# Optimization experiments

Measured on AMD Instinct MI355X. Metric: run time of the kernel, lower is better.

The kernel has to match this reference:

```python
import jax, jax.numpy as jnp
import numpy as np

I, T, Q, K, E, H = 16, 64, 196, 32, 512, 8
D = E // H


def setup_inputs() -> dict:
    key = jax.random.key(0)
    ks = jax.random.split(key, 8)
    image = jax.random.normal(ks[0], (I, Q, E), dtype=jnp.float32)
    text = jax.random.normal(ks[1], (T, K, E), dtype=jnp.float32)
    text_mask = jax.random.randint(ks[2], (T, K), 0, 2).astype(bool)
    text_mask = text_mask.at[:, 0].set(True)  # avoid fully-masked rows
    s = 1.0 / np.sqrt(D)
    Wq = jax.random.normal(ks[3], (D, D), dtype=jnp.float32) * s
    Wk = jax.random.normal(ks[4], (D, D), dtype=jnp.float32) * s
    Wv = jax.random.normal(ks[5], (D, D), dtype=jnp.float32) * s
    Wo = jax.random.normal(ks[6], (E, E), dtype=jnp.float32) * (1.0 / np.sqrt(E))
    bo = jnp.zeros((E,), dtype=jnp.float32)
    return {"image": image, "text": text, "text_mask": text_mask,
            "Wq": Wq, "Wk": Wk, "Wv": Wv, "Wo": Wo, "bo": bo}


def reference(image, text, text_mask, Wq, Wk, Wv, Wo, bo):
    i, q_len, e = image.shape
    t, k_len, _ = text.shape
    img = image.reshape(i, q_len, H, D)   # i q h d
    txt = text.reshape(t, k_len, H, D)    # t k h d
    # torch Linear: x @ W.T (bias=False for q/k/v)
    query = jnp.einsum('iqhd,ed->iqhe', img, Wq)
    key_p = jnp.einsum('tkhd,ed->tkhe', txt, Wk)
    value = jnp.einsum('tkhd,ed->tkhe', txt, Wv)
    energy = jnp.einsum('tkhd,iqhd->ithqk', key_p, query)
    neg = jnp.finfo(jnp.float32).min
    energy = jnp.where(text_mask[None, :, None, None, :], energy, neg)
    scaled = energy / (e ** 0.5)
    attention = jax.nn.softmax(scaled, axis=-1)        # over k
    text_attention = jax.nn.softmax(scaled, axis=-2)   # over q
    out = jnp.einsum('ithqk,tkhd->itqhd', attention, value)
    out = out.reshape(i, t, q_len, e)                  # i t q (h d)
    out = jnp.einsum('itqe,fe->itqf', out, Wo) + bo    # fc_out
    out = out.mean(axis=2)                             # pooling_type='mean'
    return out, attention, text_attention
```

## Files before the change

kernel.cpp:

```cpp
#include <hip/hip_runtime.h>
#include <math.h>

#define I_N 16
#define T_N 64
#define Q_N 196
#define K_N 32
#define E_N 512
#define H_N 8
#define D_N 64

#define INV_SQRT_E (0.044194173824159216f)

typedef __attribute__((ext_vector_type(8))) short bf16x8;
typedef __attribute__((ext_vector_type(4))) float f32x4;

__device__ __forceinline__ short f2bf(float x) {
    unsigned u = __builtin_bit_cast(unsigned, x);
    unsigned r = (u + 0x7fffu + ((u >> 16) & 1u)) >> 16;
    return (short)r;
}
__device__ __forceinline__ float bf2f(short s) {
    unsigned u = ((unsigned)(unsigned short)s) << 16;
    return __builtin_bit_cast(float, u);
}

__global__ __launch_bounds__(512) void detect_mask_kernel(const unsigned int* __restrict__ mask,
                                                          int* __restrict__ flag) {
    __shared__ int notSimple, sawFloat;
    int tid = threadIdx.x;
    if (tid == 0) { notSimple = 0; sawFloat = 0; }
    __syncthreads();
    unsigned int v = mask[tid];
    if (v != 0u && v != 1u && v != 0x3f800000u) atomicOr(&notSimple, 1);
    if (v == 0x3f800000u) atomicOr(&sawFloat, 1);
    __syncthreads();
    if (tid == 0) flag[0] = notSimple ? 2 : (sawFloat ? 1 : 0);
}

__global__ __launch_bounds__(256) void proj_q_kernel(const float* __restrict__ x,
                                                     const float* __restrict__ W,
                                                     unsigned short* __restrict__ qh,
                                                     unsigned short* __restrict__ ql) {
    __shared__ float sWt[64 * 65];
    __shared__ float sX[16 * 64];
    int tid = threadIdx.x;
    for (int j = tid; j < 4096; j += 256) {
        int n = j >> 6, d = j & 63;
        sWt[d * 65 + n] = W[j];
    }
    int rowBase = blockIdx.x * 16;
    for (int j = tid; j < 1024; j += 256) sX[j] = x[rowBase * 64 + j];
    __syncthreads();
    int wave = tid >> 6, lane = tid & 63;
    float acc[4] = {0.f, 0.f, 0.f, 0.f};
    for (int d = 0; d < 64; ++d) {
        float w = sWt[d * 65 + lane];
#pragma unroll
        for (int j = 0; j < 4; ++j) acc[j] += sX[(wave * 4 + j) * 64 + d] * w;
    }
#pragma unroll
    for (int j = 0; j < 4; ++j) {
        int r = rowBase + wave * 4 + j;
        int i = r / (Q_N * H_N);
        int rem = r - i * (Q_N * H_N);
        int q = rem >> 3, h = rem & 7;
        size_t dst = (((size_t)i * H_N + h) * Q_N + q) * 64 + lane;
        float a = acc[j] * INV_SQRT_E;
        short hi = f2bf(a);
        qh[dst] = (unsigned short)hi;
        ql[dst] = (unsigned short)f2bf(a - bf2f(hi));
    }
}

__global__ __launch_bounds__(256) void proj_kv_kernel(const float* __restrict__ x,
                                                      const float* __restrict__ Wk,
                                                      const float* __restrict__ Wv,
                                                      unsigned short* __restrict__ kh,
                                                      unsigned short* __restrict__ kl,
                                                      float* __restrict__ vout) {
    __shared__ float sWkT[64 * 65];
    __shared__ float sWvT[64 * 65];
    __shared__ float sX[16 * 64];
    int tid = threadIdx.x;
    for (int j = tid; j < 4096; j += 256) {
        int n = j >> 6, d = j & 63;
        sWkT[d * 65 + n] = Wk[j];
        sWvT[d * 65 + n] = Wv[j];
    }
    int rowBase = blockIdx.x * 16;
    for (int j = tid; j < 1024; j += 256) sX[j] = x[rowBase * 64 + j];
    __syncthreads();
    int wave = tid >> 6, lane = tid & 63;
    float ak[4] = {0.f, 0.f, 0.f, 0.f};
    float av[4] = {0.f, 0.f, 0.f, 0.f};
    for (int d = 0; d < 64; ++d) {
        float wk = sWkT[d * 65 + lane];
        float wv = sWvT[d * 65 + lane];
#pragma unroll
        for (int j = 0; j < 4; ++j) {
            float xv = sX[(wave * 4 + j) * 64 + d];
            ak[j] += xv * wk;
            av[j] += xv * wv;
        }
    }
#pragma unroll
    for (int j = 0; j < 4; ++j) {
        int r = rowBase + wave * 4 + j;
        int t = r >> 8;
        int rem = r & 255;
        int k = rem >> 3, h = rem & 7;
        size_t dst = (((size_t)t * H_N + h) * K_N + k) * 64 + lane;
        short hi = f2bf(ak[j]);
        kh[dst] = (unsigned short)hi;
        kl[dst] = (unsigned short)f2bf(ak[j] - bf2f(hi));
        vout[dst] = av[j];
    }
}

__global__ __launch_bounds__(256) void transpose_wo_kernel(const float* __restrict__ Wo,
                                                           float* __restrict__ WoT) {
    __shared__ float tile[32][33];
    int tx = threadIdx.x & 31, ty = threadIdx.x >> 5;
    int e0 = blockIdx.x * 32, f0 = blockIdx.y * 32;
#pragma unroll
    for (int k = 0; k < 4; ++k) {
        int fy = ty + k * 8;
        tile[fy][tx] = Wo[(size_t)(f0 + fy) * E_N + e0 + tx];
    }
    __syncthreads();
#pragma unroll
    for (int k = 0; k < 4; ++k) {
        int ey = ty + k * 8;
        WoT[(size_t)(e0 + ey) * E_N + f0 + tx] = tile[tx][ey];
    }
}

__global__ __launch_bounds__(256) void attn_kernel(const unsigned short* __restrict__ qhi,
                                                   const unsigned short* __restrict__ qlo,
                                                   const unsigned short* __restrict__ khi,
                                                   const unsigned short* __restrict__ klo,
                                                   const float* __restrict__ vproj,
                                                   const int* __restrict__ mask,
                                                   const int* __restrict__ modeFlag,
                                                   float* __restrict__ attn_out,
                                                   float* __restrict__ tattn_out,
                                                   float* __restrict__ pooled) {
    __shared__ float sS[Q_N * 33];
    __shared__ float sRrow[Q_N];
    __shared__ float sColS[4 * 32];
    __shared__ float sCaW[4 * 32];
    __shared__ float sColR[32];
    __shared__ float sCa[32];
    __shared__ float sMask[K_N];

    int tid = threadIdx.x;
    int bid = blockIdx.x;
    int h = bid & 7;
    int t = (bid >> 3) & 63;
    int i = bid >> 9;
    int lane = tid & 63, wave = tid >> 6;
    int quad = lane >> 4, lid = lane & 15;

    int mode = modeFlag[0];
    if (tid < K_N) {
        int idx = t * K_N + tid;
        bool keep;
        if (mode == 2)      keep = ((const unsigned char*)mask)[idx] != 0;
        else if (mode == 1) keep = ((const float*)mask)[idx] != 0.0f;
        else                keep = mask[idx] != 0;
        sMask[tid] = keep ? 1.0f : 0.0f;
    }
    __syncthreads();

    size_t kbase = ((size_t)t * H_N + h) * (K_N * 64);
    bf16x8 Bh[2][2], Bl[2][2];
#pragma unroll
    for (int nt = 0; nt < 2; ++nt)
#pragma unroll
        for (int ks = 0; ks < 2; ++ks) {
            size_t off = kbase + (size_t)(nt * 16 + lid) * 64 + ks * 32 + quad * 8;
            Bh[nt][ks] = *(const bf16x8*)(khi + off);
            Bl[nt][ks] = *(const bf16x8*)(klo + off);
        }

    float keep0 = sMask[lid], keep1 = sMask[16 + lid];
    size_t qoff = ((size_t)i * H_N + h) * (Q_N * 64);

    float cs0 = 0.f, cs1 = 0.f;

    for (int mt = wave; mt < 13; mt += 4) {
        int qb = mt * 16;
        int qr = qb + lid; if (qr > Q_N - 1) qr = Q_N - 1;
        const unsigned short* ph = qhi + qoff + (size_t)qr * 64 + quad * 8;
        const unsigned short* pl = qlo + qoff + (size_t)qr * 64 + quad * 8;
        bf16x8 Ah0 = *(const bf16x8*)ph;
        bf16x8 Ah1 = *(const bf16x8*)(ph + 32);
        bf16x8 Al0 = *(const bf16x8*)pl;
        bf16x8 Al1 = *(const bf16x8*)(pl + 32);

        f32x4 acc0 = {0.f, 0.f, 0.f, 0.f}, acc1 = {0.f, 0.f, 0.f, 0.f};
        acc0 = __builtin_amdgcn_mfma_f32_16x16x32_bf16(Al0, Bh[0][0], acc0, 0, 0, 0);
        acc0 = __builtin_amdgcn_mfma_f32_16x16x32_bf16(Ah0, Bl[0][0], acc0, 0, 0, 0);
        acc0 = __builtin_amdgcn_mfma_f32_16x16x32_bf16(Ah0, Bh[0][0], acc0, 0, 0, 0);
        acc0 = __builtin_amdgcn_mfma_f32_16x16x32_bf16(Al1, Bh[0][1], acc0, 0, 0, 0);
        acc0 = __builtin_amdgcn_mfma_f32_16x16x32_bf16(Ah1, Bl[0][1], acc0, 0, 0, 0);
        acc0 = __builtin_amdgcn_mfma_f32_16x16x32_bf16(Ah1, Bh[0][1], acc0, 0, 0, 0);
        acc1 = __builtin_amdgcn_mfma_f32_16x16x32_bf16(Al0, Bh[1][0], acc1, 0, 0, 0);
        acc1 = __builtin_amdgcn_mfma_f32_16x16x32_bf16(Ah0, Bl[1][0], acc1, 0, 0, 0);
        acc1 = __builtin_amdgcn_mfma_f32_16x16x32_bf16(Ah0, Bh[1][0], acc1, 0, 0, 0);
        acc1 = __builtin_amdgcn_mfma_f32_16x16x32_bf16(Al1, Bh[1][1], acc1, 0, 0, 0);
        acc1 = __builtin_amdgcn_mfma_f32_16x16x32_bf16(Ah1, Bl[1][1], acc1, 0, 0, 0);
        acc1 = __builtin_amdgcn_mfma_f32_16x16x32_bf16(Ah1, Bh[1][1], acc1, 0, 0, 0);

#pragma unroll
        for (int reg = 0; reg < 4; ++reg) {
            int q = qb + quad * 4 + reg;
            bool valid = q < Q_N;
            float p0 = keep0 * __expf(acc0[reg]);
            float p1 = keep1 * __expf(acc1[reg]);
            if (valid) {
                sS[q * 33 + lid] = p0;
                sS[q * 33 + 16 + lid] = p1;
                cs0 += p0;
                cs1 += p1;
            }
            float rs = p0 + p1;
            rs += __shfl_xor(rs, 1);
            rs += __shfl_xor(rs, 2);
            rs += __shfl_xor(rs, 4);
            rs += __shfl_xor(rs, 8);
            if (valid && lid == 0) sRrow[q] = 1.0f / rs;
        }
    }
    cs0 += __shfl_xor(cs0, 16);
    cs0 += __shfl_xor(cs0, 32);
    cs1 += __shfl_xor(cs1, 16);
    cs1 += __shfl_xor(cs1, 32);
    if (lane < 16) {
        sColS[wave * 32 + lid] = cs0;
        sColS[wave * 32 + 16 + lid] = cs1;
    }
    __syncthreads();

    if (tid < 32) {
        float s = sColS[tid] + sColS[32 + tid] + sColS[64 + tid] + sColS[96 + tid];
        sColR[tid] = s > 0.f ? 1.0f / s : -1.0f;
    }
    __syncthreads();

    const float invQ = 1.0f / 196.0f;
    int rowt = tid >> 3, kg = tid & 7;
    float cr[4];
#pragma unroll
    for (int c = 0; c < 4; ++c) cr[c] = sColR[kg * 4 + c];
    float ca[4] = {0.f, 0.f, 0.f, 0.f};
    float* ab = attn_out + (size_t)bid * (Q_N * K_N);
    float* tb = tattn_out + (size_t)bid * (Q_N * K_N);
#pragma unroll
    for (int j = 0; j < 7; ++j) {
        int qq = rowt + 32 * j;
        if (qq < Q_N) {
            float rr = sRrow[qq];
            const float* rp = &sS[qq * 33 + kg * 4];
            float p0 = rp[0], p1 = rp[1], p2 = rp[2], p3 = rp[3];
            f32x4 av = {p0 * rr, p1 * rr, p2 * rr, p3 * rr};
            ca[0] += av[0]; ca[1] += av[1]; ca[2] += av[2]; ca[3] += av[3];
            f32x4 tv = {cr[0] < 0.f ? invQ : p0 * cr[0],
                        cr[1] < 0.f ? invQ : p1 * cr[1],
                        cr[2] < 0.f ? invQ : p2 * cr[2],
                        cr[3] < 0.f ? invQ : p3 * cr[3]};
            __builtin_nontemporal_store(av, (f32x4*)(ab + qq * 32 + kg * 4));
            __builtin_nontemporal_store(tv, (f32x4*)(tb + qq * 32 + kg * 4));
        }
    }
#pragma unroll
    for (int c = 0; c < 4; ++c) {
        ca[c] += __shfl_xor(ca[c], 8);
        ca[c] += __shfl_xor(ca[c], 16);
        ca[c] += __shfl_xor(ca[c], 32);
    }
    if (lane < 8) {
#pragma unroll
        for (int c = 0; c < 4; ++c) sCaW[wave * 32 + lane * 4 + c] = ca[c];
    }
    __syncthreads();
    if (tid < 32) sCa[tid] = sCaW[tid] + sCaW[32 + tid] + sCaW[64 + tid] + sCaW[96 + tid];
    __syncthreads();

    if (tid < 64) {
        const float* vb = vproj + kbase + tid;
        float acc = 0.f;
#pragma unroll
        for (int k = 0; k < K_N; ++k) acc += sCa[k] * vb[k * 64];
        pooled[((size_t)(i * T_N + t)) * E_N + h * 64 + tid] = acc;
    }
}

__global__ __launch_bounds__(256) void fc_out_kernel(const float* __restrict__ pooled,
                                                     const float* __restrict__ WoT,
                                                     const float* __restrict__ bo,
                                                     float* __restrict__ out) {
    __shared__ float sPT[E_N * 4];
    int tid = threadIdx.x;
    int p0 = blockIdx.x * 4;
#pragma unroll
    for (int j = 0; j < 4; ++j) {
        sPT[tid * 4 + j] = pooled[(size_t)(p0 + j) * E_N + tid];
        sPT[(256 + tid) * 4 + j] = pooled[(size_t)(p0 + j) * E_N + 256 + tid];
    }
    __syncthreads();
    const float4* sPT4 = (const float4*)sPT;
    int f = blockIdx.y * 256 + tid;
    float4 acc = make_float4(0.f, 0.f, 0.f, 0.f);
    for (int e = 0; e < E_N; e += 2) {
        float w0 = WoT[(size_t)e * E_N + f];
        float w1 = WoT[(size_t)(e + 1) * E_N + f];
        float4 pv0 = sPT4[e];
        float4 pv1 = sPT4[e + 1];
        acc.x += pv0.x * w0 + pv1.x * w1;
        acc.y += pv0.y * w0 + pv1.y * w1;
        acc.z += pv0.z * w0 + pv1.z * w1;
        acc.w += pv0.w * w0 + pv1.w * w1;
    }
    const float invQ = 1.0f / 196.0f;
    float b = bo[f];
    out[(size_t)(p0 + 0) * E_N + f] = b + acc.x * invQ;
    out[(size_t)(p0 + 1) * E_N + f] = b + acc.y * invQ;
    out[(size_t)(p0 + 2) * E_N + f] = b + acc.z * invQ;
    out[(size_t)(p0 + 3) * E_N + f] = b + acc.w * invQ;
}

extern "C" void kernel_launch(void* const* d_in, const int* in_sizes, int n_in,
                              void* d_out, int out_size, void* d_ws, size_t ws_size,
                              hipStream_t stream) {
    const float* image = (const float*)d_in[0];
    const float* text  = (const float*)d_in[1];
    const int*   mask  = (const int*)d_in[2];
    const float* Wq    = (const float*)d_in[3];
    const float* Wk    = (const float*)d_in[4];
    const float* Wv    = (const float*)d_in[5];
    const float* Wo    = (const float*)d_in[6];
    const float* bo    = (const float*)d_in[7];
    float* out = (float*)d_out;

    unsigned short* qhi = (unsigned short*)d_ws;
    unsigned short* qlo = qhi + (size_t)I_N * Q_N * H_N * D_N;
    unsigned short* khi = qlo + (size_t)I_N * Q_N * H_N * D_N;
    unsigned short* klo = khi + (size_t)T_N * K_N * H_N * D_N;
    float* vproj  = (float*)(klo + (size_t)T_N * K_N * H_N * D_N);
    float* pooled = vproj + (size_t)T_N * K_N * H_N * D_N;
    float* WoT    = pooled + (size_t)I_N * T_N * E_N;
    int*   mode   = (int*)(WoT + (size_t)E_N * E_N);

    float* attn  = out + (size_t)I_N * T_N * E_N;
    float* tattn = attn + (size_t)I_N * T_N * H_N * Q_N * K_N;

    detect_mask_kernel<<<1, 512, 0, stream>>>((const unsigned int*)mask, mode);
    proj_q_kernel<<<(I_N * Q_N * H_N) / 16, 256, 0, stream>>>(image, Wq, qhi, qlo);
    proj_kv_kernel<<<(T_N * K_N * H_N) / 16, 256, 0, stream>>>(text, Wk, Wv, khi, klo, vproj);
    transpose_wo_kernel<<<dim3(16, 16), 256, 0, stream>>>(Wo, WoT);
    attn_kernel<<<I_N * T_N * H_N, 256, 0, stream>>>(qhi, qlo, khi, klo, vproj, mask, mode,
                                                     attn, tattn, pooled);
    fc_out_kernel<<<dim3((I_N * T_N) / 4, 2), 256, 0, stream>>>(pooled, WoT, bo, out);
}
```

Before: 508.3 us.

## Merge prep kernels into one launch and write attention inside softmax loop

Folds the mask detection, Q projection, K/V projection and Wo transpose into a single prep kernel that dispatches on block index, so three kernel launches go away. In the attention kernel, the row-softmax normalisation and the attention store now happen directly in the MMA/exp loop, with the column sums of attention accumulated in registers. This drops the per-row reciprocal array in shared memory and one pair of barriers. The trade-off is that attention rows are now written as scalar per-lane stores instead of f32x4 vectors. The merged kernel also reserves the largest shared-memory footprint for every block, which may lower occupancy for the Q-projection blocks.

```diff
diff --git a/kernel.cpp b/kernel.cpp
--- a/kernel.cpp
+++ b/kernel.cpp
@@ -24,114 +24,122 @@
     return __builtin_bit_cast(float, u);
 }
 
-__global__ __launch_bounds__(512) void detect_mask_kernel(const unsigned int* __restrict__ mask,
-                                                          int* __restrict__ flag) {
-    __shared__ int notSimple, sawFloat;
-    int tid = threadIdx.x;
-    if (tid == 0) { notSimple = 0; sawFloat = 0; }
-    __syncthreads();
-    unsigned int v = mask[tid];
-    if (v != 0u && v != 1u && v != 0x3f800000u) atomicOr(&notSimple, 1);
-    if (v == 0x3f800000u) atomicOr(&sawFloat, 1);
-    __syncthreads();
-    if (tid == 0) flag[0] = notSimple ? 2 : (sawFloat ? 1 : 0);
-}
-
-__global__ __launch_bounds__(256) void proj_q_kernel(const float* __restrict__ x,
-                                                     const float* __restrict__ W,
-                                                     unsigned short* __restrict__ qh,
-                                                     unsigned short* __restrict__ ql) {
-    __shared__ float sWt[64 * 65];
-    __shared__ float sX[16 * 64];
-    int tid = threadIdx.x;
-    for (int j = tid; j < 4096; j += 256) {
-        int n = j >> 6, d = j & 63;
-        sWt[d * 65 + n] = W[j];
-    }
-    int rowBase = blockIdx.x * 16;
-    for (int j = tid; j < 1024; j += 256) sX[j] = x[rowBase * 64 + j];
-    __syncthreads();
-    int wave = tid >> 6, lane = tid & 63;
-    float acc[4] = {0.f, 0.f, 0.f, 0.f};
-    for (int d = 0; d < 64; ++d) {
-        float w = sWt[d * 65 + lane];
-#pragma unroll
-        for (int j = 0; j < 4; ++j) acc[j] += sX[(wave * 4 + j) * 64 + d] * w;
-    }
-#pragma unroll
-    for (int j = 0; j < 4; ++j) {
-        int r = rowBase + wave * 4 + j;
-        int i = r / (Q_N * H_N);
-        int rem = r - i * (Q_N * H_N);
-        int q = rem >> 3, h = rem & 7;
-        size_t dst = (((size_t)i * H_N + h) * Q_N + q) * 64 + lane;
-        float a = acc[j] * INV_SQRT_E;
-        short hi = f2bf(a);
-        qh[dst] = (unsigned short)hi;
-        ql[dst] = (unsigned short)f2bf(a - bf2f(hi));
-    }
-}
-
-__global__ __launch_bounds__(256) void proj_kv_kernel(const float* __restrict__ x,
-                                                      const float* __restrict__ Wk,
-                                                      const float* __restrict__ Wv,
-                                                      unsigned short* __restrict__ kh,
-                                                      unsigned short* __restrict__ kl,
-                                                      float* __restrict__ vout) {
-    __shared__ float sWkT[64 * 65];
-    __shared__ float sWvT[64 * 65];
-    __shared__ float sX[16 * 64];
-    int tid = threadIdx.x;
-    for (int j = tid; j < 4096; j += 256) {
-        int n = j >> 6, d = j & 63;
-        sWkT[d * 65 + n] = Wk[j];
-        sWvT[d * 65 + n] = Wv[j];
-    }
-    int rowBase = blockIdx.x * 16;
-    for (int j = tid; j < 1024; j += 256) sX[j] = x[rowBase * 64 + j];
-    __syncthreads();
-    int wave = tid >> 6, lane = tid & 63;
-    float ak[4] = {0.f, 0.f, 0.f, 0.f};
-    float av[4] = {0.f, 0.f, 0.f, 0.f};
-    for (int d = 0; d < 64; ++d) {
-        float wk = sWkT[d * 65 + lane];
-        float wv = sWvT[d * 65 + lane];
+#define PQ_BLOCKS 1568
+#define PKV_BLOCKS 1024
+#define TW_BLOCKS 256
+#define PREP_GRID (PQ_BLOCKS + PKV_BLOCKS + TW_BLOCKS + 1)
+
+__global__ __launch_bounds__(256) void prep_kernel(const float* __restrict__ image,
+                                                   const float* __restrict__ Wq,
+                                                   const float* __restrict__ text,
+                                                   const float* __restrict__ Wk,
+                                                   const float* __restrict__ Wv,
+                                                   const float* __restrict__ Wo,
+                                                   const unsigned int* __restrict__ mask,
+                                                   unsigned short* __restrict__ qh,
+                                                   unsigned short* __restrict__ ql,
+                                                   unsigned short* __restrict__ kh,
+                                                   unsigned short* __restrict__ kl,
+                                                   float* __restrict__ vout,
+                                                   float* __restrict__ WoT,
+                                                   int* __restrict__ flag) {
+    __shared__ float smem[2 * 4160 + 1024];
+    int bid = blockIdx.x, tid = threadIdx.x;
+
+    if (bid < PQ_BLOCKS) {
+        float* sWt = smem;
+        float* sX  = smem + 4160;
+        for (int j = tid; j < 4096; j += 256) {
+            int n = j >> 6, d = j & 63;
+            sWt[d * 65 + n] = Wq[j];
+        }
+        int rowBase = bid * 16;
+        for (int j = tid; j < 1024; j += 256) sX[j] = image[rowBase * 64 + j];
+        __syncthreads();
+        int wave = tid >> 6, lane = tid & 63;
+        float acc[4] = {0.f, 0.f, 0.f, 0.f};
+        for (int d = 0; d < 64; ++d) {
+            float w = sWt[d * 65 + lane];
+#pragma unroll
+            for (int j = 0; j < 4; ++j) acc[j] += sX[(wave * 4 + j) * 64 + d] * w;
+        }
 #pragma unroll
         for (int j = 0; j < 4; ++j) {
-            float xv = sX[(wave * 4 + j) * 64 + d];
-            ak[j] += xv * wk;
-            av[j] += xv * wv;
-        }
-    }
-#pragma unroll
-    for (int j = 0; j < 4; ++j) {
-        int r = rowBase + wave * 4 + j;
-        int t = r >> 8;
-        int rem = r & 255;
-        int k = rem >> 3, h = rem & 7;
-        size_t dst = (((size_t)t * H_N + h) * K_N + k) * 64 + lane;
-        short hi = f2bf(ak[j]);
-        kh[dst] = (unsigned short)hi;
-        kl[dst] = (unsigned short)f2bf(ak[j] - bf2f(hi));
-        vout[dst] = av[j];
-    }
-}
-
-__global__ __launch_bounds__(256) void transpose_wo_kernel(const float* __restrict__ Wo,
-                                                           float* __restrict__ WoT) {
-    __shared__ float tile[32][33];
-    int tx = threadIdx.x & 31, ty = threadIdx.x >> 5;
-    int e0 = blockIdx.x * 32, f0 = blockIdx.y * 32;
-#pragma unroll
-    for (int k = 0; k < 4; ++k) {
-        int fy = ty + k * 8;
-        tile[fy][tx] = Wo[(size_t)(f0 + fy) * E_N + e0 + tx];
-    }
-    __syncthreads();
-#pragma unroll
-    for (int k = 0; k < 4; ++k) {
-        int ey = ty + k * 8;
-        WoT[(size_t)(e0 + ey) * E_N + f0 + tx] = tile[tx][ey];
+            int r = rowBase + wave * 4 + j;
+            int i = r / (Q_N * H_N);
+            int rem = r - i * (Q_N * H_N);
+            int q = rem >> 3, h = rem & 7;
+            size_t dst = (((size_t)i * H_N + h) * Q_N + q) * 64 + lane;
+            float a = acc[j] * INV_SQRT_E;
+            short hi = f2bf(a);
+            qh[dst] = (unsigned short)hi;
+            ql[dst] = (unsigned short)f2bf(a - bf2f(hi));
+        }
+    } else if (bid < PQ_BLOCKS + PKV_BLOCKS) {
+        float* sWkT = smem;
+        float* sWvT = smem + 4160;
+        float* sX   = smem + 8320;
+        for (int j = tid; j < 4096; j += 256) {
+            int n = j >> 6, d = j & 63;
+            sWkT[d * 65 + n] = Wk[j];
+            sWvT[d * 65 + n] = Wv[j];
+        }
+        int rowBase = (bid - PQ_BLOCKS) * 16;
+        for (int j = tid; j < 1024; j += 256) sX[j] = text[rowBase * 64 + j];
+        __syncthreads();
+        int wave = tid >> 6, lane = tid & 63;
+        float ak[4] = {0.f, 0.f, 0.f, 0.f};
+        float av[4] = {0.f, 0.f, 0.f, 0.f};
+        for (int d = 0; d < 64; ++d) {
+            float wk = sWkT[d * 65 + lane];
+            float wv = sWvT[d * 65 + lane];
+#pragma unroll
+            for (int j = 0; j < 4; ++j) {
+                float xv = sX[(wave * 4 + j) * 64 + d];
+                ak[j] += xv * wk;
+                av[j] += xv * wv;
+            }
+        }
+#pragma unroll
+        for (int j = 0; j < 4; ++j) {
+            int r = rowBase + wave * 4 + j;
+            int t = r >> 8;
+            int rem = r & 255;
+            int k = rem >> 3, h = rem & 7;
+            size_t dst = (((size_t)t * H_N + h) * K_N + k) * 64 + lane;
+            short hi = f2bf(ak[j]);
+            kh[dst] = (unsigned short)hi;
+            kl[dst] = (unsigned short)f2bf(ak[j] - bf2f(hi));
+            vout[dst] = av[j];
+        }
+    } else if (bid < PQ_BLOCKS + PKV_BLOCKS + TW_BLOCKS) {
+        float (*tile)[33] = (float (*)[33])smem;
+        int b = bid - (PQ_BLOCKS + PKV_BLOCKS);
+        int tx = tid & 31, ty = tid >> 5;
+        int e0 = (b & 15) * 32, f0 = (b >> 4) * 32;
+#pragma unroll
+        for (int k = 0; k < 4; ++k) {
+            int fy = ty + k * 8;
+            tile[fy][tx] = Wo[(size_t)(f0 + fy) * E_N + e0 + tx];
+        }
+        __syncthreads();
+#pragma unroll
+        for (int k = 0; k < 4; ++k) {
+            int ey = ty + k * 8;
+            WoT[(size_t)(e0 + ey) * E_N + f0 + tx] = tile[tx][ey];
+        }
+    } else {
+        int* fl = (int*)smem;
+        if (tid == 0) { fl[0] = 0; fl[1] = 0; }
+        __syncthreads();
+#pragma unroll
+        for (int j = 0; j < 2; ++j) {
+            unsigned int v = mask[tid + j * 256];
+            if (v != 0u && v != 1u && v != 0x3f800000u) atomicOr(&fl[0], 1);
+            if (v == 0x3f800000u) atomicOr(&fl[1], 1);
+        }
+        __syncthreads();
+        if (tid == 0) flag[0] = fl[0] ? 2 : (fl[1] ? 1 : 0);
     }
 }
 
@@ -146,7 +154,6 @@
                                                    float* __restrict__ tattn_out,
                                                    float* __restrict__ pooled) {
     __shared__ float sS[Q_N * 33];
-    __shared__ float sRrow[Q_N];
     __shared__ float sColS[4 * 32];
     __shared__ float sCaW[4 * 32];
     __shared__ float sColR[32];
@@ -185,8 +192,10 @@
 
     float keep0 = sMask[lid], keep1 = sMask[16 + lid];
     size_t qoff = ((size_t)i * H_N + h) * (Q_N * 64);
+    float* ab = attn_out + (size_t)bid * (Q_N * K_N);
 
     float cs0 = 0.f, cs1 = 0.f;
+    float ca0 = 0.f, ca1 = 0.f;
 
     for (int mt = wave; mt < 13; mt += 4) {
         int qb = mt * 16;
@@ -218,33 +227,41 @@
             bool valid = q < Q_N;
             float p0 = keep0 * __expf(acc0[reg]);
             float p1 = keep1 * __expf(acc1[reg]);
+            float rs = p0 + p1;
+            rs += __shfl_xor(rs, 1);
+            rs += __shfl_xor(rs, 2);
+            rs += __shfl_xor(rs, 4);
+            rs += __shfl_xor(rs, 8);
+            float rr = 1.0f / rs;
             if (valid) {
                 sS[q * 33 + lid] = p0;
                 sS[q * 33 + 16 + lid] = p1;
                 cs0 += p0;
                 cs1 += p1;
+                float a0 = p0 * rr, a1 = p1 * rr;
+                ca0 += a0;
+                ca1 += a1;
+                __builtin_nontemporal_store(a0, ab + q * 32 + lid);
+                __builtin_nontemporal_store(a1, ab + q * 32 + 16 + lid);
             }
-            float rs = p0 + p1;
-            rs += __shfl_xor(rs, 1);
-            rs += __shfl_xor(rs, 2);
-            rs += __shfl_xor(rs, 4);
-            rs += __shfl_xor(rs, 8);
-            if (valid && lid == 0) sRrow[q] = 1.0f / rs;
-        }
-    }
-    cs0 += __shfl_xor(cs0, 16);
-    cs0 += __shfl_xor(cs0, 32);
-    cs1 += __shfl_xor(cs1, 16);
-    cs1 += __shfl_xor(cs1, 32);
+        }
+    }
+    cs0 += __shfl_xor(cs0, 16);  cs0 += __shfl_xor(cs0, 32);
+    cs1 += __shfl_xor(cs1, 16);  cs1 += __shfl_xor(cs1, 32);
+    ca0 += __shfl_xor(ca0, 16);  ca0 += __shfl_xor(ca0, 32);
+    ca1 += __shfl_xor(ca1, 16);  ca1 += __shfl_xor(ca1, 32);
     if (lane < 16) {
         sColS[wave * 32 + lid] = cs0;
         sColS[wave * 32 + 16 + lid] = cs1;
+        sCaW[wave * 32 + lid] = ca0;
+        sCaW[wave * 32 + 16 + lid] = ca1;
     }
     __syncthreads();
 
     if (tid < 32) {
         float s = sColS[tid] + sColS[32 + tid] + sColS[64 + tid] + sColS[96 + tid];
         sColR[tid] = s > 0.f ? 1.0f / s : -1.0f;
+        sCa[tid] = sCaW[tid] + sCaW[32 + tid] + sCaW[64 + tid] + sCaW[96 + tid];
     }
     __syncthreads();
 
@@ -253,39 +270,20 @@
     float cr[4];
 #pragma unroll
     for (int c = 0; c < 4; ++c) cr[c] = sColR[kg * 4 + c];
-    float ca[4] = {0.f, 0.f, 0.f, 0.f};
-    float* ab = attn_out + (size_t)bid * (Q_N * K_N);
     float* tb = tattn_out + (size_t)bid * (Q_N * K_N);
 #pragma unroll
     for (int j = 0; j < 7; ++j) {
         int qq = rowt + 32 * j;
         if (qq < Q_N) {
-            float rr = sRrow[qq];
             const float* rp = &sS[qq * 33 + kg * 4];
             float p0 = rp[0], p1 = rp[1], p2 = rp[2], p3 = rp[3];
-            f32x4 av = {p0 * rr, p1 * rr, p2 * rr, p3 * rr};
-            ca[0] += av[0]; ca[1] += av[1]; ca[2] += av[2]; ca[3] += av[3];
             f32x4 tv = {cr[0] < 0.f ? invQ : p0 * cr[0],
                         cr[1] < 0.f ? invQ : p1 * cr[1],
                         cr[2] < 0.f ? invQ : p2 * cr[2],
                         cr[3] < 0.f ? invQ : p3 * cr[3]};
-            __builtin_nontemporal_store(av, (f32x4*)(ab + qq * 32 + kg * 4));
             __builtin_nontemporal_store(tv, (f32x4*)(tb + qq * 32 + kg * 4));
         }
     }
-#pragma unroll
-    for (int c = 0; c < 4; ++c) {
-        ca[c] += __shfl_xor(ca[c], 8);
-        ca[c] += __shfl_xor(ca[c], 16);
-        ca[c] += __shfl_xor(ca[c], 32);
-    }
-    if (lane < 8) {
-#pragma unroll
-        for (int c = 0; c < 4; ++c) sCaW[wave * 32 + lane * 4 + c] = ca[c];
-    }
-    __syncthreads();
-    if (tid < 32) sCa[tid] = sCaW[tid] + sCaW[32 + tid] + sCaW[64 + tid] + sCaW[96 + tid];
-    __syncthreads();
 
     if (tid < 64) {
         const float* vb = vproj + kbase + tid;
@@ -355,10 +353,9 @@
     float* attn  = out + (size_t)I_N * T_N * E_N;
     float* tattn = attn + (size_t)I_N * T_N * H_N * Q_N * K_N;
 
-    detect_mask_kernel<<<1, 512, 0, stream>>>((const unsigned int*)mask, mode);
-    proj_q_kernel<<<(I_N * Q_N * H_N) / 16, 256, 0, stream>>>(image, Wq, qhi, qlo);
-    proj_kv_kernel<<<(T_N * K_N * H_N) / 16, 256, 0, stream>>>(text, Wk, Wv, khi, klo, vproj);
-    transpose_wo_kernel<<<dim3(16, 16), 256, 0, stream>>>(Wo, WoT);
+    prep_kernel<<<PREP_GRID, 256, 0, stream>>>(image, Wq, text, Wk, Wv, Wo,
+                                               (const unsigned int*)mask,
+                                               qhi, qlo, khi, klo, vproj, WoT, mode);
     attn_kernel<<<I_N * T_N * H_N, 256, 0, stream>>>(qhi, qlo, khi, klo, vproj, mask, mode,
                                                      attn, tattn, pooled);
     fc_out_kernel<<<dim3((I_N * T_N) / 4, 2), 256, 0, stream>>>(pooled, WoT, bo, out);
```

Measured after the change: 496.6 us. 2.3% less time.
